# Performance work log

Measured on AMD Instinct MI355X. Metric: run time of the kernel, lower is better.

Reference implementation:

```python
import jax, jax.numpy as jnp
import numpy as np

NUM_PTS = 8   # num_points_per_face
K = 5         # self.k


def _sq_dist(x, y):
    # squared euclidean distance matrix (Nx, Ny); matches torch.cdist**2 / sum((a-b)**2)
    x2 = jnp.sum(x * x, axis=1)[:, None]
    y2 = jnp.sum(y * y, axis=1)[None, :]
    d = x2 + y2 - 2.0 * (x @ y.T)
    return jnp.maximum(d, 0.0)


def setup_inputs() -> dict:
    key = jax.random.key(0)
    k1, k2, k3, k4, k5, k6, k7 = jax.random.split(key, 7)
    V, Fs, Ft = 2048, 4096, 4096
    return {
        "source_vertices": jax.random.normal(k1, (1, V, 3), dtype=jnp.float32),
        "source_faces": jax.random.randint(k2, (Fs, 3), 0, V),
        "target_vertices": jax.random.normal(k3, (1, V, 3), dtype=jnp.float32),
        "target_faces": jax.random.randint(k4, (3, Ft), 0, V),
        "face_probs": jax.random.uniform(k5, (Fs,), dtype=jnp.float32),
        "r1u": jax.random.uniform(k6, (Fs, NUM_PTS), dtype=jnp.float32),
        "r2u": jax.random.uniform(k7, (Fs, NUM_PTS), dtype=jnp.float32),
    }


def reference(source_vertices, source_faces, target_vertices, target_faces, face_probs, r1u, r2u):
    sv = source_vertices[0]                 # (V, 3)
    tv = target_vertices[0]                 # (V, 3)
    tf = target_faces.T                     # (Ft, 3)
    Fs = source_faces.shape[0]

    src_bc = sv[source_faces].mean(axis=1)  # (Fs, 3) source barycenters
    tgt_bc = tv[tf].mean(axis=1)            # (Ft, 3) target barycenters

    # ---- forward loss: prob-weighted min squared distance to target barycenters
    d_fwd = _sq_dist(src_bc, tgt_bc)        # (Fs, Ft)
    forward_loss = jnp.sum(face_probs * jnp.min(d_fwd, axis=1))

    # ---- sample points from triangles via barycentric coords
    r1 = jnp.sqrt(r1u)
    w1 = 1.0 - r1
    w2 = r1 * (1.0 - r2u)
    w3 = r1 * r2u
    v1 = sv[source_faces[:, 0]]             # (Fs, 3)
    v2 = sv[source_faces[:, 1]]
    v3 = sv[source_faces[:, 2]]
    pts = (w1[..., None] * v1[:, None] + w2[..., None] * v2[:, None]
           + w3[..., None] * v3[:, None]).reshape(-1, 3)   # (P, 3), P = Fs*NUM_PTS
    pt_faces = jnp.repeat(jnp.arange(Fs), NUM_PTS)          # (P,)
    pt_probs = face_probs[pt_faces]                         # (P,)

    # ---- reverse loss, batched over all P points
    d_src = _sq_dist(pts, src_bc)                           # (P, Fs)
    neg_d, idx = jax.lax.top_k(-d_src, K + 1)               # K+1 smallest distances
    tri_dists = -neg_d                                      # (P, K+1)
    mask = idx != pt_faces[:, None]                         # exclude own face
    has_self = jnp.any(~mask, axis=1)
    excl_pos = jnp.where(has_self, jnp.argmin(mask, axis=1), K + 1)  # (P,)
    t = jnp.arange(K)
    sel = t[None, :] + (t[None, :] >= excl_pos[:, None]).astype(jnp.int32)  # (P, K)
    valid_dists = jnp.take_along_axis(tri_dists, sel, axis=1)   # (P, K)
    valid_idx = jnp.take_along_axis(idx, sel, axis=1)           # (P, K)
    valid_probs = face_probs[valid_idx]                         # (P, K)

    min_tgt = jnp.min(_sq_dist(pts, tgt_bc), axis=1)            # (P,)

    reverse_loss = jnp.sum(pt_probs * min_tgt
                           + (1.0 - pt_probs) * jnp.mean(valid_probs * valid_dists, axis=1))
    return forward_loss + reverse_loss
```

## Files before the change

### kernel.cpp

```cpp
#include <hip/hip_runtime.h>
#include <math.h>

#define FS 4096
#define FT 4096
#define TS 256
#define NPH 16
#define BIGF 3.0e38f
#define KEYINF 0xFFFFFFFFu

typedef float v2f __attribute__((ext_vector_type(2)));

__device__ __forceinline__ unsigned umin32(unsigned a, unsigned b) { return a < b ? a : b; }
__device__ __forceinline__ unsigned umax32(unsigned a, unsigned b) { return a < b ? b : a; }

__device__ __forceinline__ unsigned med3u(unsigned a, unsigned b, unsigned c) {
    unsigned d;
    asm("v_med3_u32 %0, %1, %2, %3" : "=v"(d) : "v"(a), "v"(b), "v"(c));
    return d;
}

__device__ __forceinline__ unsigned and_or(unsigned a, unsigned m, unsigned o) {
    unsigned d;
    asm("v_and_or_b32 %0, %1, %2, %3" : "=v"(d) : "v"(a), "v"(m), "v"(o));
    return d;
}

__device__ __forceinline__ v2f pk_add(v2f a, v2f b) {
    v2f d;
    asm("v_pk_add_f32 %0, %1, %2" : "=v"(d) : "v"(a), "v"(b));
    return d;
}
__device__ __forceinline__ v2f pk_fma(v2f a, v2f b, v2f c) {
    v2f d;
    asm("v_pk_fma_f32 %0, %1, %2, %3" : "=v"(d) : "v"(a), "v"(b), "v"(c));
    return d;
}
__device__ __forceinline__ void pk_fma_acc(v2f& d, v2f a, v2f b) {
    asm("v_pk_fma_f32 %0, %1, %2, %0" : "+v"(d) : "v"(a), "v"(b));
}

__device__ __forceinline__ void gl_lds16(const float4* g, float4* l) {
    __builtin_amdgcn_global_load_lds(
        (__attribute__((address_space(1))) void*)(g),
        (__attribute__((address_space(3))) void*)(l), 16, 0, 0);
}

__device__ __forceinline__ float block_reduce_sum(float v) {
    __shared__ float s[8];
    for (int o = 32; o > 0; o >>= 1) v += __shfl_down(v, o, 64);
    int lane = threadIdx.x & 63, wid = threadIdx.x >> 6;
    if (lane == 0) s[wid] = v;
    __syncthreads();
    int nw = blockDim.x >> 6;
    v = (threadIdx.x < (unsigned)nw) ? s[threadIdx.x] : 0.f;
    if (wid == 0)
        for (int o = 4; o > 0; o >>= 1) v += __shfl_down(v, o, 64);
    return v;
}

#define CE(x, y) { unsigned _n = umin32(x, y); y = umax32(x, y); x = _n; }

__device__ __forceinline__ void merge32(unsigned s[6]) {
    #pragma unroll
    for (int m = 1; m <= 16; m <<= 1) {
        unsigned b0 = __shfl_xor(s[0], m, 64), b1 = __shfl_xor(s[1], m, 64);
        unsigned b2 = __shfl_xor(s[2], m, 64), b3 = __shfl_xor(s[3], m, 64);
        unsigned b4 = __shfl_xor(s[4], m, 64), b5 = __shfl_xor(s[5], m, 64);
        unsigned l0 = s[0], l1 = s[1];
        unsigned l2 = umin32(s[2], b5), l3 = umin32(s[3], b4);
        unsigned l4 = umin32(s[4], b3), l5 = umin32(s[5], b2);
        unsigned l6 = b1, l7 = b0;
        CE(l0, l4) CE(l1, l5) CE(l2, l6) CE(l3, l7)
        CE(l0, l2) CE(l1, l3) CE(l4, l6) CE(l5, l7)
        CE(l0, l1) CE(l2, l3) CE(l4, l5) CE(l6, l7)
        s[0] = l0; s[1] = l1; s[2] = l2; s[3] = l3; s[4] = l4; s[5] = l5;
    }
}

__global__ __launch_bounds__(64) void k_prep(
        const float* __restrict__ sv, const int* __restrict__ sf,
        const float* __restrict__ tv, const int* __restrict__ tf,
        float4* __restrict__ sbc2, float4* __restrict__ tbc2,
        float4* __restrict__ sbcr, float* __restrict__ out) {
    int i = blockIdx.x * 64 + threadIdx.x;
    if (i == 0) out[0] = 0.f;
    if (i >= FS) return;
    const float third = 1.f / 3.f;
    int a = sf[3*i], b = sf[3*i+1], c = sf[3*i+2];
    float x = (sv[3*a  ] + sv[3*b  ] + sv[3*c  ]) * third;
    float y = (sv[3*a+1] + sv[3*b+1] + sv[3*c+1]) * third;
    float z = (sv[3*a+2] + sv[3*b+2] + sv[3*c+2]) * third;
    float n2 = x*x + y*y + z*z;
    sbcr[i] = make_float4(x, y, z, n2);
    int ta = tf[i], tb = tf[FT + i], tc = tf[2*FT + i];
    float tx = (tv[3*ta  ] + tv[3*tb  ] + tv[3*tc  ]) * third;
    float ty = (tv[3*ta+1] + tv[3*tb+1] + tv[3*tc+1]) * third;
    float tz = (tv[3*ta+2] + tv[3*tb+2] + tv[3*tc+2]) * third;
    float tn2 = tx*tx + ty*ty + tz*tz;

    int tt = i >> 10, cc = i & 1023;
    int g = cc >> 6, half = (cc >> 5) & 1, pp = cc & 31;
    int lo4 = tt*1024 + g*32 + pp, hi4 = lo4 + 512;
    float* S = (float*)sbc2;
    S[4*lo4 + half]     = -2.f*x;  S[4*lo4 + 2 + half] = -2.f*y;
    S[4*hi4 + half]     = -2.f*z;  S[4*hi4 + 2 + half] = n2;
    float* T = (float*)tbc2;
    T[4*lo4 + half]     = -2.f*tx; T[4*lo4 + 2 + half] = -2.f*ty;
    T[4*hi4 + half]     = -2.f*tz; T[4*hi4 + 2 + half] = tn2;
}

#define STAGE_OFF(p) ((((p) >> 2) << 10) + (((p) & 3) << 7) + (tid & 127) + ((tid >> 7) << 9))

__global__ __launch_bounds__(256, 4) void k_main(
        const float* __restrict__ sv, const int* __restrict__ sf,
        const float* __restrict__ fp,
        const float* __restrict__ r1u, const float* __restrict__ r2u,
        const float4* __restrict__ sbc2, const float4* __restrict__ tbc2,
        const float4* __restrict__ sbcr, float* __restrict__ out) {
    __shared__ float4 tileS[2][TS];
    __shared__ float4 tileT[2][TS];
    int tid  = threadIdx.x;
    int seg  = tid & 31;
    int slot = tid >> 5;
    float contrib = 0.f;

    if (blockIdx.x < 1024) {
        int pt0  = blockIdx.x * 32 + slot * 4;
        int face = pt0 >> 3;

        int a = sf[3*face], b = sf[3*face+1], c = sf[3*face+2];
        float ax = sv[3*a], ay = sv[3*a+1], az = sv[3*a+2];
        float bx = sv[3*b], by = sv[3*b+1], bz = sv[3*b+2];
        float cx = sv[3*c], cy = sv[3*c+1], cz = sv[3*c+2];
        float4 r14 = ((const float4*)r1u)[pt0 >> 2];
        float4 r24 = ((const float4*)r2u)[pt0 >> 2];
        v2f pxb[4], pyb[4], pzb[4], p2b[4];
        {
            float r1a[4] = {r14.x, r14.y, r14.z, r14.w};
            float r2a[4] = {r24.x, r24.y, r24.z, r24.w};
            #pragma unroll
            for (int i = 0; i < 4; ++i) {
                float r1 = sqrtf(r1a[i]);
                float w1 = 1.f - r1, w2 = r1 * (1.f - r2a[i]), w3 = r1 * r2a[i];
                float px = w1*ax + w2*bx + w3*cx;
                float py = w1*ay + w2*by + w3*cy;
                float pz = w1*az + w2*bz + w3*cz;
                float p2 = px*px + py*py + pz*pz;
                pxb[i] = (v2f){px, px}; pyb[i] = (v2f){py, py};
                pzb[i] = (v2f){pz, pz}; p2b[i] = (v2f){p2, p2};
            }
        }

        unsigned s0[4], s1[4], s2[4];
        #pragma unroll
        for (int i = 0; i < 4; ++i) { s0[i]=KEYINF; s1[i]=KEYINF; s2[i]=KEYINF; }
        v2f vm2[4];
        #pragma unroll
        for (int i = 0; i < 4; ++i) vm2[i] = (v2f){BIGF, BIGF};

        unsigned kMask = 0xFFFFF000u;

        {
            int off = STAGE_OFF(0);
            gl_lds16(&sbc2[off], &tileS[0][tid]);
            gl_lds16(&tbc2[off], &tileT[0][tid]);
        }

        for (int p = 0; p < NPH; ++p) {
            int buf = p & 1;
            __syncthreads();
            if (p + 1 < NPH) {
                int off = STAGE_OFF(p + 1);
                gl_lds16(&sbc2[off], &tileS[buf ^ 1][tid]);
                gl_lds16(&tbc2[off], &tileT[buf ^ 1][tid]);
            }
            unsigned jja = (unsigned)(p * TS + seg);
            #pragma unroll
            for (int jp = 0; jp < 4; ++jp) {
                float4 lo = tileS[buf][(jp << 5) + seg];
                float4 hi = tileS[buf][128 + (jp << 5) + seg];
                v2f cx2 = {lo.x, lo.y}, cy2 = {lo.z, lo.w};
                v2f cz2 = {hi.x, hi.y}, cw2 = {hi.z, hi.w};
                #pragma unroll
                for (int i = 0; i < 4; ++i) {
                    v2f d2 = pk_add(cw2, p2b[i]);
                    pk_fma_acc(d2, pzb[i], cz2);
                    pk_fma_acc(d2, pyb[i], cy2);
                    pk_fma_acc(d2, pxb[i], cx2);
                    unsigned ka = and_or(__float_as_uint(d2.x), kMask, jja);
                    unsigned kb = and_or(__float_as_uint(d2.y), kMask, jja + 32u);
                    unsigned n0 = umin32(s0[i], ka);
                    unsigned n1 = med3u(s0[i], s1[i], ka);
                    unsigned n2 = med3u(s1[i], s2[i], ka);
                    s0[i]=n0; s1[i]=n1; s2[i]=n2;
                    n0 = umin32(s0[i], kb);
                    n1 = med3u(s0[i], s1[i], kb);
                    n2 = med3u(s1[i], s2[i], kb);
                    s0[i]=n0; s1[i]=n1; s2[i]=n2;
                }
                jja += 64;
            }
            #pragma unroll
            for (int jp = 0; jp < 4; ++jp) {
                float4 lo = tileT[buf][(jp << 5) + seg];
                float4 hi = tileT[buf][128 + (jp << 5) + seg];
                v2f cx2 = {lo.x, lo.y}, cy2 = {lo.z, lo.w};
                v2f cz2 = {hi.x, hi.y}, cw2 = {hi.z, hi.w};
                #pragma unroll
                for (int i = 0; i < 4; ++i) {
                    v2f t = pk_fma(pzb[i], cz2, cw2);
                    pk_fma_acc(t, pyb[i], cy2);
                    pk_fma_acc(t, pxb[i], cx2);
                    vm2[i].x = fminf(vm2[i].x, t.x);
                    vm2[i].y = fminf(vm2[i].y, t.y);
                }
            }
        }

        float vm[4];
        #pragma unroll
        for (int i = 0; i < 4; ++i) {
            float v = fminf(vm2[i].x, vm2[i].y);
            v = fminf(v, __shfl_xor(v, 1, 64));
            v = fminf(v, __shfl_xor(v, 2, 64));
            v = fminf(v, __shfl_xor(v, 4, 64));
            v = fminf(v, __shfl_xor(v, 8, 64));
            v = fminf(v, __shfl_xor(v, 16, 64));
            vm[i] = v;
        }

        float pf = fp[face];
        float csum = 0.f;
        #pragma unroll
        for (int i = 0; i < 4; ++i) {
            unsigned srt[6] = {s0[i], s1[i], s2[i], KEYINF, KEYINF, KEYINF};
            merge32(srt);
            if (seg == 0) {
                int   q0 = srt[0] & 0xFFF, q1 = srt[1] & 0xFFF, q2 = srt[2] & 0xFFF;
                int   q3 = srt[3] & 0xFFF, q4 = srt[4] & 0xFFF, q5 = srt[5] & 0xFFF;
                float d0 = __uint_as_float(srt[0] & 0xFFFFF000u);
                float d1 = __uint_as_float(srt[1] & 0xFFFFF000u);
                float d2 = __uint_as_float(srt[2] & 0xFFFFF000u);
                float d3 = __uint_as_float(srt[3] & 0xFFFFF000u);
                float d4 = __uint_as_float(srt[4] & 0xFFFFF000u);
                float d5 = __uint_as_float(srt[5] & 0xFFFFF000u);

                int skip = 5;
                if      (q0 == face) skip = 0;
                else if (q1 == face) skip = 1;
                else if (q2 == face) skip = 2;
                else if (q3 == face) skip = 3;
                else if (q4 == face) skip = 4;

                float s = 0.f;
                if (skip != 0) s += fp[q0] * d0;
                if (skip != 1) s += fp[q1] * d1;
                if (skip != 2) s += fp[q2] * d2;
                if (skip != 3) s += fp[q3] * d3;
                if (skip != 4) s += fp[q4] * d4;
                if (skip != 5) s += fp[q5] * d5;

                float mtd = fmaxf(vm[i] + p2b[i].x, 0.f);
                csum += pf * mtd + (1.f - pf) * (s * 0.2f);
            }
        }
        if (seg == 0) contrib = csum;
    } else {
        int f0 = (blockIdx.x - 1024) * 32 + slot * 4;
        float qw[4];
        v2f qxb[4], qyb[4], qzb[4];
        #pragma unroll
        for (int i = 0; i < 4; ++i) {
            float4 q = sbcr[f0 + i];
            qxb[i] = (v2f){q.x, q.x}; qyb[i] = (v2f){q.y, q.y};
            qzb[i] = (v2f){q.z, q.z}; qw[i] = q.w;
        }
        v2f vf2[4];
        #pragma unroll
        for (int i = 0; i < 4; ++i) vf2[i] = (v2f){BIGF, BIGF};

        {
            int off = STAGE_OFF(0);
            gl_lds16(&tbc2[off], &tileT[0][tid]);
        }
        for (int p = 0; p < NPH; ++p) {
            int buf = p & 1;
            __syncthreads();
            if (p + 1 < NPH) {
                int off = STAGE_OFF(p + 1);
                gl_lds16(&tbc2[off], &tileT[buf ^ 1][tid]);
            }
            #pragma unroll
            for (int jp = 0; jp < 4; ++jp) {
                float4 lo = tileT[buf][(jp << 5) + seg];
                float4 hi = tileT[buf][128 + (jp << 5) + seg];
                v2f cx2 = {lo.x, lo.y}, cy2 = {lo.z, lo.w};
                v2f cz2 = {hi.x, hi.y}, cw2 = {hi.z, hi.w};
                #pragma unroll
                for (int i = 0; i < 4; ++i) {
                    v2f t = pk_fma(qzb[i], cz2, cw2);
                    pk_fma_acc(t, qyb[i], cy2);
                    pk_fma_acc(t, qxb[i], cx2);
                    vf2[i].x = fminf(vf2[i].x, t.x);
                    vf2[i].y = fminf(vf2[i].y, t.y);
                }
            }
        }
        float vf[4];
        #pragma unroll
        for (int i = 0; i < 4; ++i) {
            float v = fminf(vf2[i].x, vf2[i].y);
            v = fminf(v, __shfl_xor(v, 1, 64));
            v = fminf(v, __shfl_xor(v, 2, 64));
            v = fminf(v, __shfl_xor(v, 4, 64));
            v = fminf(v, __shfl_xor(v, 8, 64));
            v = fminf(v, __shfl_xor(v, 16, 64));
            vf[i] = v;
        }
        if (seg == 0)
            contrib = fp[f0  ] * fmaxf(vf[0] + qw[0], 0.f)
                    + fp[f0+1] * fmaxf(vf[1] + qw[1], 0.f)
                    + fp[f0+2] * fmaxf(vf[2] + qw[2], 0.f)
                    + fp[f0+3] * fmaxf(vf[3] + qw[3], 0.f);
    }

    float tot = block_reduce_sum(contrib);
    if (tid == 0) atomicAdd(out, tot);
}

extern "C" void kernel_launch(void* const* d_in, const int* in_sizes, int n_in,
                              void* d_out, int out_size, void* d_ws, size_t ws_size,
                              hipStream_t stream) {
    const float* sv  = (const float*)d_in[0];
    const int*   sf  = (const int*)  d_in[1];
    const float* tv  = (const float*)d_in[2];
    const int*   tf  = (const int*)  d_in[3];
    const float* fp  = (const float*)d_in[4];
    const float* r1u = (const float*)d_in[5];
    const float* r2u = (const float*)d_in[6];
    float* out = (float*)d_out;

    char* ws = (char*)d_ws;
    float4* sbc2 = (float4*)(ws);
    float4* tbc2 = (float4*)(ws + 65536);
    float4* sbcr = (float4*)(ws + 131072);

    k_prep<<<64,   64,  0, stream>>>(sv, sf, tv, tf, sbc2, tbc2, sbcr, out);
    k_main<<<1152, 256, 0, stream>>>(sv, sf, fp, r1u, r2u, sbc2, tbc2, sbcr, out);
}
```

Measured before the change: 114.8 us.

## Halve block size to 128 threads and drop LDS double buffering

```diff
diff --git a/kernel.cpp b/kernel.cpp
--- a/kernel.cpp
+++ b/kernel.cpp
@@ -5,6 +5,7 @@
 #define FT 4096
 #define TS 256
 #define NPH 16
+#define REVB 2048
 #define BIGF 3.0e38f
 #define KEYINF 0xFFFFFFFFu
 
@@ -109,23 +110,21 @@
     T[4*hi4 + half]     = -2.f*tz; T[4*hi4 + 2 + half] = tn2;
 }
 
-#define STAGE_OFF(p) ((((p) >> 2) << 10) + (((p) & 3) << 7) + (tid & 127) + ((tid >> 7) << 9))
-
-__global__ __launch_bounds__(256, 4) void k_main(
+__global__ __launch_bounds__(128, 4) void k_main(
         const float* __restrict__ sv, const int* __restrict__ sf,
         const float* __restrict__ fp,
         const float* __restrict__ r1u, const float* __restrict__ r2u,
         const float4* __restrict__ sbc2, const float4* __restrict__ tbc2,
         const float4* __restrict__ sbcr, float* __restrict__ out) {
-    __shared__ float4 tileS[2][TS];
-    __shared__ float4 tileT[2][TS];
+    __shared__ float4 tileS[TS];
+    __shared__ float4 tileT[TS];
     int tid  = threadIdx.x;
     int seg  = tid & 31;
     int slot = tid >> 5;
     float contrib = 0.f;
 
-    if (blockIdx.x < 1024) {
-        int pt0  = blockIdx.x * 32 + slot * 4;
+    if (blockIdx.x < REVB) {
+        int pt0  = blockIdx.x * 16 + slot * 4;
         int face = pt0 >> 3;
 
         int a = sf[3*face], b = sf[3*face+1], c = sf[3*face+2];
@@ -160,25 +159,19 @@
 
         unsigned kMask = 0xFFFFF000u;
 
-        {
-            int off = STAGE_OFF(0);
-            gl_lds16(&sbc2[off], &tileS[0][tid]);
-            gl_lds16(&tbc2[off], &tileT[0][tid]);
-        }
-
         for (int p = 0; p < NPH; ++p) {
-            int buf = p & 1;
+            int b0 = ((p >> 2) << 10) + ((p & 3) << 7);
             __syncthreads();
-            if (p + 1 < NPH) {
-                int off = STAGE_OFF(p + 1);
-                gl_lds16(&sbc2[off], &tileS[buf ^ 1][tid]);
-                gl_lds16(&tbc2[off], &tileT[buf ^ 1][tid]);
-            }
+            gl_lds16(&sbc2[b0 + tid],       &tileS[tid]);
+            gl_lds16(&sbc2[b0 + 512 + tid], &tileS[128 + tid]);
+            gl_lds16(&tbc2[b0 + tid],       &tileT[tid]);
+            gl_lds16(&tbc2[b0 + 512 + tid], &tileT[128 + tid]);
+            __syncthreads();
             unsigned jja = (unsigned)(p * TS + seg);
             #pragma unroll
             for (int jp = 0; jp < 4; ++jp) {
-                float4 lo = tileS[buf][(jp << 5) + seg];
-                float4 hi = tileS[buf][128 + (jp << 5) + seg];
+                float4 lo = tileS[(jp << 5) + seg];
+                float4 hi = tileS[128 + (jp << 5) + seg];
                 v2f cx2 = {lo.x, lo.y}, cy2 = {lo.z, lo.w};
                 v2f cz2 = {hi.x, hi.y}, cw2 = {hi.z, hi.w};
                 #pragma unroll
@@ -202,8 +195,8 @@
             }
             #pragma unroll
             for (int jp = 0; jp < 4; ++jp) {
-                float4 lo = tileT[buf][(jp << 5) + seg];
-                float4 hi = tileT[buf][128 + (jp << 5) + seg];
+                float4 lo = tileT[(jp << 5) + seg];
+                float4 hi = tileT[128 + (jp << 5) + seg];
                 v2f cx2 = {lo.x, lo.y}, cy2 = {lo.z, lo.w};
                 v2f cz2 = {hi.x, hi.y}, cw2 = {hi.z, hi.w};
                 #pragma unroll
@@ -266,7 +259,7 @@
         }
         if (seg == 0) contrib = csum;
     } else {
-        int f0 = (blockIdx.x - 1024) * 32 + slot * 4;
+        int f0 = (blockIdx.x - REVB) * 16 + slot * 4;
         float qw[4];
         v2f qxb[4], qyb[4], qzb[4];
         #pragma unroll
@@ -279,21 +272,16 @@
         #pragma unroll
         for (int i = 0; i < 4; ++i) vf2[i] = (v2f){BIGF, BIGF};
 
-        {
-            int off = STAGE_OFF(0);
-            gl_lds16(&tbc2[off], &tileT[0][tid]);
-        }
         for (int p = 0; p < NPH; ++p) {
-            int buf = p & 1;
+            int b0 = ((p >> 2) << 10) + ((p & 3) << 7);
             __syncthreads();
-            if (p + 1 < NPH) {
-                int off = STAGE_OFF(p + 1);
-                gl_lds16(&tbc2[off], &tileT[buf ^ 1][tid]);
-            }
+            gl_lds16(&tbc2[b0 + tid],       &tileT[tid]);
+            gl_lds16(&tbc2[b0 + 512 + tid], &tileT[128 + tid]);
+            __syncthreads();
             #pragma unroll
             for (int jp = 0; jp < 4; ++jp) {
-                float4 lo = tileT[buf][(jp << 5) + seg];
-                float4 hi = tileT[buf][128 + (jp << 5) + seg];
+                float4 lo = tileT[(jp << 5) + seg];
+                float4 hi = tileT[128 + (jp << 5) + seg];
                 v2f cx2 = {lo.x, lo.y}, cy2 = {lo.z, lo.w};
                 v2f cz2 = {hi.x, hi.y}, cw2 = {hi.z, hi.w};
                 #pragma unroll
@@ -346,5 +334,5 @@
     float4* sbcr = (float4*)(ws + 131072);
 
     k_prep<<<64,   64,  0, stream>>>(sv, sf, tv, tf, sbc2, tbc2, sbcr, out);
-    k_main<<<1152, 256, 0, stream>>>(sv, sf, fp, r1u, r2u, sbc2, tbc2, sbcr, out);
-}
+    k_main<<<2304, 128, 0, stream>>>(sv, sf, fp, r1u, r2u, sbc2, tbc2, sbcr, out);
+}
```

Result: slower. 129.4 us (+12.7%).

## Replace LDS double-buffered staging with direct global loads of centroid tiles

Applied to the files above, without the earlier changes.

```diff
diff --git a/kernel.cpp b/kernel.cpp
--- a/kernel.cpp
+++ b/kernel.cpp
@@ -3,8 +3,6 @@
 
 #define FS 4096
 #define FT 4096
-#define TS 256
-#define NPH 16
 #define BIGF 3.0e38f
 #define KEYINF 0xFFFFFFFFu
 
@@ -37,12 +35,6 @@
 }
 __device__ __forceinline__ void pk_fma_acc(v2f& d, v2f a, v2f b) {
     asm("v_pk_fma_f32 %0, %1, %2, %0" : "+v"(d) : "v"(a), "v"(b));
-}
-
-__device__ __forceinline__ void gl_lds16(const float4* g, float4* l) {
-    __builtin_amdgcn_global_load_lds(
-        (__attribute__((address_space(1))) void*)(g),
-        (__attribute__((address_space(3))) void*)(l), 16, 0, 0);
 }
 
 __device__ __forceinline__ float block_reduce_sum(float v) {
@@ -109,16 +101,12 @@
     T[4*hi4 + half]     = -2.f*tz; T[4*hi4 + 2 + half] = tn2;
 }
 
-#define STAGE_OFF(p) ((((p) >> 2) << 10) + (((p) & 3) << 7) + (tid & 127) + ((tid >> 7) << 9))
-
-__global__ __launch_bounds__(256, 4) void k_main(
+__global__ __launch_bounds__(256) void k_main(
         const float* __restrict__ sv, const int* __restrict__ sf,
         const float* __restrict__ fp,
         const float* __restrict__ r1u, const float* __restrict__ r2u,
         const float4* __restrict__ sbc2, const float4* __restrict__ tbc2,
         const float4* __restrict__ sbcr, float* __restrict__ out) {
-    __shared__ float4 tileS[2][TS];
-    __shared__ float4 tileT[2][TS];
     int tid  = threadIdx.x;
     int seg  = tid & 31;
     int slot = tid >> 5;
@@ -160,60 +148,50 @@
 
         unsigned kMask = 0xFFFFF000u;
 
-        {
-            int off = STAGE_OFF(0);
-            gl_lds16(&sbc2[off], &tileS[0][tid]);
-            gl_lds16(&tbc2[off], &tileT[0][tid]);
-        }
-
-        for (int p = 0; p < NPH; ++p) {
-            int buf = p & 1;
-            __syncthreads();
-            if (p + 1 < NPH) {
-                int off = STAGE_OFF(p + 1);
-                gl_lds16(&sbc2[off], &tileS[buf ^ 1][tid]);
-                gl_lds16(&tbc2[off], &tileT[buf ^ 1][tid]);
-            }
-            unsigned jja = (unsigned)(p * TS + seg);
-            #pragma unroll
-            for (int jp = 0; jp < 4; ++jp) {
-                float4 lo = tileS[buf][(jp << 5) + seg];
-                float4 hi = tileS[buf][128 + (jp << 5) + seg];
-                v2f cx2 = {lo.x, lo.y}, cy2 = {lo.z, lo.w};
-                v2f cz2 = {hi.x, hi.y}, cw2 = {hi.z, hi.w};
-                #pragma unroll
-                for (int i = 0; i < 4; ++i) {
-                    v2f d2 = pk_add(cw2, p2b[i]);
-                    pk_fma_acc(d2, pzb[i], cz2);
-                    pk_fma_acc(d2, pyb[i], cy2);
-                    pk_fma_acc(d2, pxb[i], cx2);
-                    unsigned ka = and_or(__float_as_uint(d2.x), kMask, jja);
-                    unsigned kb = and_or(__float_as_uint(d2.y), kMask, jja + 32u);
-                    unsigned n0 = umin32(s0[i], ka);
-                    unsigned n1 = med3u(s0[i], s1[i], ka);
-                    unsigned n2 = med3u(s1[i], s2[i], ka);
-                    s0[i]=n0; s1[i]=n1; s2[i]=n2;
-                    n0 = umin32(s0[i], kb);
-                    n1 = med3u(s0[i], s1[i], kb);
-                    n2 = med3u(s1[i], s2[i], kb);
-                    s0[i]=n0; s1[i]=n1; s2[i]=n2;
+        for (int tt = 0; tt < 4; ++tt) {
+            const float4* Sb = sbc2 + (tt << 10) + seg;
+            const float4* Tb = tbc2 + (tt << 10) + seg;
+            unsigned jja = (unsigned)((tt << 10) + seg);
+            #pragma unroll 4
+            for (int g = 0; g < 16; ++g) {
+                float4 slo = Sb[(g << 5)];
+                float4 shi = Sb[(g << 5) + 512];
+                float4 tlo = Tb[(g << 5)];
+                float4 thi = Tb[(g << 5) + 512];
+                {
+                    v2f cx2 = {slo.x, slo.y}, cy2 = {slo.z, slo.w};
+                    v2f cz2 = {shi.x, shi.y}, cw2 = {shi.z, shi.w};
+                    #pragma unroll
+                    for (int i = 0; i < 4; ++i) {
+                        v2f d2 = pk_add(cw2, p2b[i]);
+                        pk_fma_acc(d2, pzb[i], cz2);
+                        pk_fma_acc(d2, pyb[i], cy2);
+                        pk_fma_acc(d2, pxb[i], cx2);
+                        unsigned ka = and_or(__float_as_uint(d2.x), kMask, jja);
+                        unsigned kb = and_or(__float_as_uint(d2.y), kMask, jja + 32u);
+                        unsigned n0 = umin32(s0[i], ka);
+                        unsigned n1 = med3u(s0[i], s1[i], ka);
+                        unsigned n2 = med3u(s1[i], s2[i], ka);
+                        s0[i]=n0; s1[i]=n1; s2[i]=n2;
+                        n0 = umin32(s0[i], kb);
+                        n1 = med3u(s0[i], s1[i], kb);
+                        n2 = med3u(s1[i], s2[i], kb);
+                        s0[i]=n0; s1[i]=n1; s2[i]=n2;
+                    }
+                }
+                {
+                    v2f cx2 = {tlo.x, tlo.y}, cy2 = {tlo.z, tlo.w};
+                    v2f cz2 = {thi.x, thi.y}, cw2 = {thi.z, thi.w};
+                    #pragma unroll
+                    for (int i = 0; i < 4; ++i) {
+                        v2f t = pk_fma(pzb[i], cz2, cw2);
+                        pk_fma_acc(t, pyb[i], cy2);
+                        pk_fma_acc(t, pxb[i], cx2);
+                        vm2[i].x = fminf(vm2[i].x, t.x);
+                        vm2[i].y = fminf(vm2[i].y, t.y);
+                    }
                 }
                 jja += 64;
-            }
-            #pragma unroll
-            for (int jp = 0; jp < 4; ++jp) {
-                float4 lo = tileT[buf][(jp << 5) + seg];
-                float4 hi = tileT[buf][128 + (jp << 5) + seg];
-                v2f cx2 = {lo.x, lo.y}, cy2 = {lo.z, lo.w};
-                v2f cz2 = {hi.x, hi.y}, cw2 = {hi.z, hi.w};
-                #pragma unroll
-                for (int i = 0; i < 4; ++i) {
-                    v2f t = pk_fma(pzb[i], cz2, cw2);
-                    pk_fma_acc(t, pyb[i], cy2);
-                    pk_fma_acc(t, pxb[i], cx2);
-                    vm2[i].x = fminf(vm2[i].x, t.x);
-                    vm2[i].y = fminf(vm2[i].y, t.y);
-                }
             }
         }
 
@@ -279,23 +257,14 @@
         #pragma unroll
         for (int i = 0; i < 4; ++i) vf2[i] = (v2f){BIGF, BIGF};
 
-        {
-            int off = STAGE_OFF(0);
-            gl_lds16(&tbc2[off], &tileT[0][tid]);
-        }
-        for (int p = 0; p < NPH; ++p) {
-            int buf = p & 1;
-            __syncthreads();
-            if (p + 1 < NPH) {
-                int off = STAGE_OFF(p + 1);
-                gl_lds16(&tbc2[off], &tileT[buf ^ 1][tid]);
-            }
-            #pragma unroll
-            for (int jp = 0; jp < 4; ++jp) {
-                float4 lo = tileT[buf][(jp << 5) + seg];
-                float4 hi = tileT[buf][128 + (jp << 5) + seg];
-                v2f cx2 = {lo.x, lo.y}, cy2 = {lo.z, lo.w};
-                v2f cz2 = {hi.x, hi.y}, cw2 = {hi.z, hi.w};
+        for (int tt = 0; tt < 4; ++tt) {
+            const float4* Tb = tbc2 + (tt << 10) + seg;
+            #pragma unroll 4
+            for (int g = 0; g < 16; ++g) {
+                float4 tlo = Tb[(g << 5)];
+                float4 thi = Tb[(g << 5) + 512];
+                v2f cx2 = {tlo.x, tlo.y}, cy2 = {tlo.z, tlo.w};
+                v2f cz2 = {thi.x, thi.y}, cw2 = {thi.z, thi.w};
                 #pragma unroll
                 for (int i = 0; i < 4; ++i) {
                     v2f t = pk_fma(qzb[i], cz2, cw2);
```

New measurement: 151.0 us. +31.5%, slower.
